# Kernel optimization log

Measured on AMD Instinct MI355X. Metric: run time of the kernel, lower is better.

Reference implementation:

```python
import jax, jax.numpy as jnp
import numpy as np

MARGIN = 1.0
EPS = 1e-08


def setup_inputs() -> dict:
    key = jax.random.key(0)
    k0, k1 = jax.random.split(key)
    kernels0 = jax.random.normal(k0, (2048, 3, 3), dtype=jnp.float32)
    kernels1 = jax.random.normal(k1, (1024, 5, 5), dtype=jnp.float32)
    return {"kernels0": kernels0, "kernels1": kernels1}


def _layer_loss(kernels):
    n, d, _ = kernels.shape
    # Frobenius-normalize each kernel
    norms = jnp.sqrt(jnp.sum(kernels * kernels, axis=(1, 2), keepdims=True)) + EPS
    kn = kernels / norms                      # (n, d, d)
    inv = jnp.linalg.inv(kn)                  # (n, d, d)
    # AB[i, j] = inv[i] @ kn[j]; BA[i, j] = inv[j] @ kn[i]
    ab = jnp.einsum('iab,jbc->ijac', inv, kn)  # (n, n, d, d)
    ba = jnp.einsum('jab,ibc->ijac', inv, kn)  # (n, n, d, d)
    eye = jnp.eye(d, dtype=kernels.dtype)
    diff_ab = jnp.sqrt(jnp.sum((eye - ab) ** 2, axis=(2, 3)))  # (n, n)
    diff_ba = jnp.sqrt(jnp.sum((eye - ba) ** 2, axis=(2, 3)))  # (n, n)
    combined = jnp.tril(diff_ab) + jnp.triu(diff_ba)
    loss_mat = jax.nn.relu(MARGIN - combined)
    mask = ~jnp.eye(n, dtype=bool)
    loss_mat = jnp.where(mask, loss_mat, 0.0)
    return jnp.sum(loss_mat) / (n * (n - 1))


def reference(kernels0, kernels1):
    losses = [_layer_loss(kernels0), _layer_loss(kernels1)]
    return sum(losses) / len(losses)
```

## Files before the change

kernel.cpp:

```cpp
#include <hip/hip_runtime.h>
#include <math.h>

#define N0 2048
#define N1 1024
#define M0T 32
#define M1T 32
#define NB0 (M0T * (M0T + 1) / 2)
#define NB1 (M1T * (M1T + 1) / 2)
#define NBLK0 (2 * NB0)
#define NBLK1 (2 * NB1)
#define NBTOT (NBLK0 + NBLK1)


__global__ __launch_bounds__(64) void prep_kernel(const float* __restrict__ k0,
                                                  const float* __restrict__ k1,
                                                  float* __restrict__ kn0,
                                                  float* __restrict__ inv0,
                                                  float* __restrict__ kn1,
                                                  float* __restrict__ inv1) {
    int t = blockIdx.x * blockDim.x + threadIdx.x;
    if (t < N0) {
        float a[9];
        float ss = 0.0f;
#pragma unroll
        for (int e = 0; e < 9; ++e) { a[e] = k0[t * 9 + e]; ss = fmaf(a[e], a[e], ss); }
        float rn = 1.0f / (sqrtf(ss) + 1e-8f);
#pragma unroll
        for (int e = 0; e < 9; ++e) a[e] *= rn;
        float c00 = a[4] * a[8] - a[5] * a[7];
        float c01 = -(a[3] * a[8] - a[5] * a[6]);
        float c02 = a[3] * a[7] - a[4] * a[6];
        float det = a[0] * c00 + a[1] * c01 + a[2] * c02;
        float id = 1.0f / det;
        float x[9];
        x[0] = c00 * id;
        x[1] = (a[2] * a[7] - a[1] * a[8]) * id;
        x[2] = (a[1] * a[5] - a[2] * a[4]) * id;
        x[3] = c01 * id;
        x[4] = (a[0] * a[8] - a[2] * a[6]) * id;
        x[5] = (a[2] * a[3] - a[0] * a[5]) * id;
        x[6] = c02 * id;
        x[7] = (a[1] * a[6] - a[0] * a[7]) * id;
        x[8] = (a[0] * a[4] - a[1] * a[3]) * id;
        float r[9];
#pragma unroll
        for (int i = 0; i < 3; ++i)
#pragma unroll
            for (int j = 0; j < 3; ++j) {
                float m = a[i * 3 + 0] * x[0 * 3 + j];
                m = fmaf(a[i * 3 + 1], x[1 * 3 + j], m);
                m = fmaf(a[i * 3 + 2], x[2 * 3 + j], m);
                r[i * 3 + j] = ((i == j) ? 2.0f : 0.0f) - m;
            }
        float xn[9];
#pragma unroll
        for (int i = 0; i < 3; ++i)
#pragma unroll
            for (int j = 0; j < 3; ++j) {
                float m = x[i * 3 + 0] * r[0 * 3 + j];
                m = fmaf(x[i * 3 + 1], r[1 * 3 + j], m);
                m = fmaf(x[i * 3 + 2], r[2 * 3 + j], m);
                xn[i * 3 + j] = m;
            }
#pragma unroll
        for (int e = 0; e < 9; ++e) {
            kn0[t * 9 + e] = a[e];
            inv0[t * 9 + e] = xn[e];
        }
    } else {
        int u = t - N0;
        if (u < N1) {
            float A[5][5], B[5][5], K[5][5];
            float ss = 0.0f;
#pragma unroll
            for (int r = 0; r < 5; ++r)
#pragma unroll
                for (int c = 0; c < 5; ++c) {
                    float v = k1[u * 25 + r * 5 + c];
                    A[r][c] = v;
                    ss = fmaf(v, v, ss);
                }
            float rn = 1.0f / (sqrtf(ss) + 1e-8f);
#pragma unroll
            for (int r = 0; r < 5; ++r)
#pragma unroll
                for (int c = 0; c < 5; ++c) {
                    A[r][c] *= rn;
                    K[r][c] = A[r][c];
                    kn1[u * 25 + r * 5 + c] = A[r][c];
                    B[r][c] = (r == c) ? 1.0f : 0.0f;
                }
#pragma unroll
            for (int k = 0; k < 5; ++k) {
#pragma unroll
                for (int r = k + 1; r < 5; ++r) {
                    bool sw = fabsf(A[r][k]) > fabsf(A[k][k]);
#pragma unroll
                    for (int c = k; c < 5; ++c) {
                        float Ar = A[r][c], Ak = A[k][c];
                        A[r][c] = sw ? Ak : Ar;
                        A[k][c] = sw ? Ar : Ak;
                    }
#pragma unroll
                    for (int c = 0; c < 5; ++c) {
                        float Br = B[r][c], Bk = B[k][c];
                        B[r][c] = sw ? Bk : Br;
                        B[k][c] = sw ? Br : Bk;
                    }
                }
                float piv = 1.0f / A[k][k];
#pragma unroll
                for (int c = k; c < 5; ++c) A[k][c] *= piv;
#pragma unroll
                for (int c = 0; c < 5; ++c) B[k][c] *= piv;
#pragma unroll
                for (int r = 0; r < 5; ++r) {
                    if (r == k) continue;
                    float f = A[r][k];
#pragma unroll
                    for (int c = k; c < 5; ++c) A[r][c] = fmaf(-f, A[k][c], A[r][c]);
#pragma unroll
                    for (int c = 0; c < 5; ++c) B[r][c] = fmaf(-f, B[k][c], B[r][c]);
                }
            }
            float R[5][5];
#pragma unroll
            for (int i = 0; i < 5; ++i)
#pragma unroll
                for (int j = 0; j < 5; ++j) {
                    float m = K[i][0] * B[0][j];
#pragma unroll
                    for (int k = 1; k < 5; ++k) m = fmaf(K[i][k], B[k][j], m);
                    R[i][j] = ((i == j) ? 2.0f : 0.0f) - m;
                }
#pragma unroll
            for (int i = 0; i < 5; ++i)
#pragma unroll
                for (int j = 0; j < 5; ++j) {
                    float m = B[i][0] * R[0][j];
#pragma unroll
                    for (int k = 1; k < 5; ++k) m = fmaf(B[i][k], R[k][j], m);
                    inv1[u * 25 + i * 5 + j] = m;
                }
        }
    }
}

__device__ __forceinline__ void tri_decode(int t, int& bi, int& bj) {
    int b = (int)((sqrtf(8.0f * t + 1.0f) - 1.0f) * 0.5f);
    while ((b + 1) * (b + 2) / 2 <= t) ++b;
    while (b * (b + 1) / 2 > t) --b;
    bi = b;
    bj = t - b * (b + 1) / 2;
}

__global__ __launch_bounds__(256) void pairs_kernel(const float* __restrict__ inv0,
                                                    const float* __restrict__ kn0,
                                                    const float* __restrict__ inv1,
                                                    const float* __restrict__ kn1,
                                                    float* __restrict__ partial) {
    __shared__ __align__(16) float sA[800];
    __shared__ __align__(16) float sB[400];
    int tid = threadIdx.x;
    float contrib = 0.0f;

    if (blockIdx.x < NBLK0) {
        int t = blockIdx.x;
        int pb = t >> 1, h = t & 1;
        int bi, bj;
        tri_decode(pb, bi, bj);

        const float4* gA = (const float4*)(inv0 + bi * 576);
        const float4* gB = (const float4*)(kn0 + bj * 576 + h * 288);
        if (tid < 216) {
            if (tid < 144) ((float4*)sA)[tid] = gA[tid];
            else ((float4*)sB)[tid - 144] = gB[tid - 144];
        }
        __syncthreads();

        int ti = tid >> 4, tj = tid & 15;
        int ibase = bi * 64 + ti * 4;
        int jbase = bj * 64 + h * 32 + tj * 2;
        float a[4][9];
#pragma unroll
        for (int u = 0; u < 4; ++u)
#pragma unroll
            for (int e = 0; e < 9; ++e) a[u][e] = sA[(ti * 4 + u) * 9 + e];
#pragma unroll
        for (int v = 0; v < 2; ++v) {
            float b[9];
#pragma unroll
            for (int e = 0; e < 9; ++e) b[e] = sB[(tj * 2 + v) * 9 + e];
#pragma unroll
            for (int u = 0; u < 4; ++u) {
                float s = 0.0f;
#pragma unroll
                for (int r = 0; r < 3; ++r)
#pragma unroll
                    for (int c = 0; c < 3; ++c) {
                        float m = a[u][r * 3 + 0] * b[c];
                        m = fmaf(a[u][r * 3 + 1], b[3 + c], m);
                        m = fmaf(a[u][r * 3 + 2], b[6 + c], m);
                        float d = ((r == c) ? 1.0f : 0.0f) - m;
                        s = fmaf(d, d, s);
                    }
                bool take = ((ibase + u) > (jbase + v)) && (s < 1.0f);
                contrib += take ? (1.0f - __builtin_amdgcn_sqrtf(s)) : 0.0f;
            }
        }
    } else {
        int t = blockIdx.x - NBLK0;
        int pb = t >> 1, h = t & 1;
        int bi, bj;
        tri_decode(pb, bi, bj);

        const float4* gA = (const float4*)(inv1 + bi * 800);
        const float4* gB = (const float4*)(kn1 + (bj * 32 + h * 16) * 25);
        for (int e = tid; e < 300; e += 256) {
            if (e < 200) ((float4*)sA)[e] = gA[e];
            else ((float4*)sB)[e - 200] = gB[e - 200];
        }
        __syncthreads();

        int ti = tid >> 4, tj = tid & 15;
        int ibase = bi * 32 + ti * 2;
        int j = bj * 32 + h * 16 + tj;
        float a[2][25];
#pragma unroll
        for (int u = 0; u < 2; ++u)
#pragma unroll
            for (int e = 0; e < 25; ++e) a[u][e] = sA[(ti * 2 + u) * 25 + e];
        float b[25];
#pragma unroll
        for (int e = 0; e < 25; ++e) b[e] = sB[tj * 25 + e];
#pragma unroll
        for (int u = 0; u < 2; ++u) {
            float s = 0.0f;
#pragma unroll
            for (int r = 0; r < 5; ++r)
#pragma unroll
                for (int c = 0; c < 5; ++c) {
                    float m = a[u][r * 5 + 0] * b[c];
#pragma unroll
                    for (int k = 1; k < 5; ++k) m = fmaf(a[u][r * 5 + k], b[k * 5 + c], m);
                    float d = ((r == c) ? 1.0f : 0.0f) - m;
                    s = fmaf(d, d, s);
                }
            bool take = ((ibase + u) > j) && (s < 1.0f);
            contrib += take ? (1.0f - __builtin_amdgcn_sqrtf(s)) : 0.0f;
        }
    }

#pragma unroll
    for (int off = 32; off; off >>= 1) contrib += __shfl_down(contrib, off);
    __shared__ float wsum[4];
    if ((tid & 63) == 0) wsum[tid >> 6] = contrib;
    __syncthreads();
    if (tid == 0) partial[blockIdx.x] = wsum[0] + wsum[1] + wsum[2] + wsum[3];
}

__global__ void finalize_kernel(const float* __restrict__ partial, float* __restrict__ out) {
    int tid = threadIdx.x;
    double s0 = 0.0, s1 = 0.0;
    for (int x = tid; x < NBLK0; x += 256) s0 += (double)partial[x];
    for (int x = NBLK0 + tid; x < NBTOT; x += 256) s1 += (double)partial[x];
#pragma unroll
    for (int off = 32; off; off >>= 1) {
        s0 += __shfl_down(s0, off);
        s1 += __shfl_down(s1, off);
    }
    __shared__ double w0[4], w1[4];
    if ((tid & 63) == 0) { w0[tid >> 6] = s0; w1[tid >> 6] = s1; }
    __syncthreads();
    if (tid == 0) {
        double S0 = w0[0] + w0[1] + w0[2] + w0[3];
        double S1 = w1[0] + w1[1] + w1[2] + w1[3];
        double res = S0 / ((double)N0 * (double)(N0 - 1)) +
                     S1 / ((double)N1 * (double)(N1 - 1));
        out[0] = (float)res;
    }
}

extern "C" void kernel_launch(void* const* d_in, const int* in_sizes, int n_in,
                              void* d_out, int out_size, void* d_ws, size_t ws_size,
                              hipStream_t stream) {
    const float* k0 = (const float*)d_in[0];
    const float* k1 = (const float*)d_in[1];
    float* out = (float*)d_out;

    float* ws = (float*)d_ws;
    float* kn0 = ws;
    float* inv0 = kn0 + N0 * 9;
    float* kn1 = inv0 + N0 * 9;
    float* inv1 = kn1 + N1 * 25;
    float* partial = inv1 + N1 * 25;

    int totalPrep = N0 + N1;
    prep_kernel<<<(totalPrep + 63) / 64, 64, 0, stream>>>(k0, k1, kn0, inv0, kn1, inv1);
    pairs_kernel<<<NBTOT, 256, 0, stream>>>(inv0, kn0, inv1, kn1, partial);
    finalize_kernel<<<1, 256, 0, stream>>>(partial, out);
}
```

Baseline: 69.82 us.

## Fuse normalization and inversion prep into the pairwise kernel, dropping prep launch

Removes the separate prep kernel and computes per-kernel normalization and inverse inside each pairs block while it loads its tiles into shared memory. This removes one kernel launch and the global round-trip for the normalized and inverted matrices. In exchange, every tile's inverses are recomputed redundantly by each block that uses them, and only a subset of threads does that serial inversion work before the barrier, which lengthens each block's prologue.

```diff
diff --git a/kernel.cpp b/kernel.cpp
--- a/kernel.cpp
+++ b/kernel.cpp
@@ -12,140 +12,6 @@
 #define NBTOT (NBLK0 + NBLK1)
 
 
-__global__ __launch_bounds__(64) void prep_kernel(const float* __restrict__ k0,
-                                                  const float* __restrict__ k1,
-                                                  float* __restrict__ kn0,
-                                                  float* __restrict__ inv0,
-                                                  float* __restrict__ kn1,
-                                                  float* __restrict__ inv1) {
-    int t = blockIdx.x * blockDim.x + threadIdx.x;
-    if (t < N0) {
-        float a[9];
-        float ss = 0.0f;
-#pragma unroll
-        for (int e = 0; e < 9; ++e) { a[e] = k0[t * 9 + e]; ss = fmaf(a[e], a[e], ss); }
-        float rn = 1.0f / (sqrtf(ss) + 1e-8f);
-#pragma unroll
-        for (int e = 0; e < 9; ++e) a[e] *= rn;
-        float c00 = a[4] * a[8] - a[5] * a[7];
-        float c01 = -(a[3] * a[8] - a[5] * a[6]);
-        float c02 = a[3] * a[7] - a[4] * a[6];
-        float det = a[0] * c00 + a[1] * c01 + a[2] * c02;
-        float id = 1.0f / det;
-        float x[9];
-        x[0] = c00 * id;
-        x[1] = (a[2] * a[7] - a[1] * a[8]) * id;
-        x[2] = (a[1] * a[5] - a[2] * a[4]) * id;
-        x[3] = c01 * id;
-        x[4] = (a[0] * a[8] - a[2] * a[6]) * id;
-        x[5] = (a[2] * a[3] - a[0] * a[5]) * id;
-        x[6] = c02 * id;
-        x[7] = (a[1] * a[6] - a[0] * a[7]) * id;
-        x[8] = (a[0] * a[4] - a[1] * a[3]) * id;
-        float r[9];
-#pragma unroll
-        for (int i = 0; i < 3; ++i)
-#pragma unroll
-            for (int j = 0; j < 3; ++j) {
-                float m = a[i * 3 + 0] * x[0 * 3 + j];
-                m = fmaf(a[i * 3 + 1], x[1 * 3 + j], m);
-                m = fmaf(a[i * 3 + 2], x[2 * 3 + j], m);
-                r[i * 3 + j] = ((i == j) ? 2.0f : 0.0f) - m;
-            }
-        float xn[9];
-#pragma unroll
-        for (int i = 0; i < 3; ++i)
-#pragma unroll
-            for (int j = 0; j < 3; ++j) {
-                float m = x[i * 3 + 0] * r[0 * 3 + j];
-                m = fmaf(x[i * 3 + 1], r[1 * 3 + j], m);
-                m = fmaf(x[i * 3 + 2], r[2 * 3 + j], m);
-                xn[i * 3 + j] = m;
-            }
-#pragma unroll
-        for (int e = 0; e < 9; ++e) {
-            kn0[t * 9 + e] = a[e];
-            inv0[t * 9 + e] = xn[e];
-        }
-    } else {
-        int u = t - N0;
-        if (u < N1) {
-            float A[5][5], B[5][5], K[5][5];
-            float ss = 0.0f;
-#pragma unroll
-            for (int r = 0; r < 5; ++r)
-#pragma unroll
-                for (int c = 0; c < 5; ++c) {
-                    float v = k1[u * 25 + r * 5 + c];
-                    A[r][c] = v;
-                    ss = fmaf(v, v, ss);
-                }
-            float rn = 1.0f / (sqrtf(ss) + 1e-8f);
-#pragma unroll
-            for (int r = 0; r < 5; ++r)
-#pragma unroll
-                for (int c = 0; c < 5; ++c) {
-                    A[r][c] *= rn;
-                    K[r][c] = A[r][c];
-                    kn1[u * 25 + r * 5 + c] = A[r][c];
-                    B[r][c] = (r == c) ? 1.0f : 0.0f;
-                }
-#pragma unroll
-            for (int k = 0; k < 5; ++k) {
-#pragma unroll
-                for (int r = k + 1; r < 5; ++r) {
-                    bool sw = fabsf(A[r][k]) > fabsf(A[k][k]);
-#pragma unroll
-                    for (int c = k; c < 5; ++c) {
-                        float Ar = A[r][c], Ak = A[k][c];
-                        A[r][c] = sw ? Ak : Ar;
-                        A[k][c] = sw ? Ar : Ak;
-                    }
-#pragma unroll
-                    for (int c = 0; c < 5; ++c) {
-                        float Br = B[r][c], Bk = B[k][c];
-                        B[r][c] = sw ? Bk : Br;
-                        B[k][c] = sw ? Br : Bk;
-                    }
-                }
-                float piv = 1.0f / A[k][k];
-#pragma unroll
-                for (int c = k; c < 5; ++c) A[k][c] *= piv;
-#pragma unroll
-                for (int c = 0; c < 5; ++c) B[k][c] *= piv;
-#pragma unroll
-                for (int r = 0; r < 5; ++r) {
-                    if (r == k) continue;
-                    float f = A[r][k];
-#pragma unroll
-                    for (int c = k; c < 5; ++c) A[r][c] = fmaf(-f, A[k][c], A[r][c]);
-#pragma unroll
-                    for (int c = 0; c < 5; ++c) B[r][c] = fmaf(-f, B[k][c], B[r][c]);
-                }
-            }
-            float R[5][5];
-#pragma unroll
-            for (int i = 0; i < 5; ++i)
-#pragma unroll
-                for (int j = 0; j < 5; ++j) {
-                    float m = K[i][0] * B[0][j];
-#pragma unroll
-                    for (int k = 1; k < 5; ++k) m = fmaf(K[i][k], B[k][j], m);
-                    R[i][j] = ((i == j) ? 2.0f : 0.0f) - m;
-                }
-#pragma unroll
-            for (int i = 0; i < 5; ++i)
-#pragma unroll
-                for (int j = 0; j < 5; ++j) {
-                    float m = B[i][0] * R[0][j];
-#pragma unroll
-                    for (int k = 1; k < 5; ++k) m = fmaf(B[i][k], R[k][j], m);
-                    inv1[u * 25 + i * 5 + j] = m;
-                }
-        }
-    }
-}
-
 __device__ __forceinline__ void tri_decode(int t, int& bi, int& bj) {
     int b = (int)((sqrtf(8.0f * t + 1.0f) - 1.0f) * 0.5f);
     while ((b + 1) * (b + 2) / 2 <= t) ++b;
@@ -154,10 +20,146 @@
     bj = t - b * (b + 1) / 2;
 }
 
-__global__ __launch_bounds__(256) void pairs_kernel(const float* __restrict__ inv0,
-                                                    const float* __restrict__ kn0,
-                                                    const float* __restrict__ inv1,
-                                                    const float* __restrict__ kn1,
+__device__ __forceinline__ void inv3_to(const float* __restrict__ g, float* __restrict__ dst) {
+    float a[9];
+    float ss = 0.0f;
+#pragma unroll
+    for (int e = 0; e < 9; ++e) { a[e] = g[e]; ss = fmaf(a[e], a[e], ss); }
+    float rn = 1.0f / (sqrtf(ss) + 1e-8f);
+#pragma unroll
+    for (int e = 0; e < 9; ++e) a[e] *= rn;
+    float c00 = a[4] * a[8] - a[5] * a[7];
+    float c01 = -(a[3] * a[8] - a[5] * a[6]);
+    float c02 = a[3] * a[7] - a[4] * a[6];
+    float det = a[0] * c00 + a[1] * c01 + a[2] * c02;
+    float id = 1.0f / det;
+    float x[9];
+    x[0] = c00 * id;
+    x[1] = (a[2] * a[7] - a[1] * a[8]) * id;
+    x[2] = (a[1] * a[5] - a[2] * a[4]) * id;
+    x[3] = c01 * id;
+    x[4] = (a[0] * a[8] - a[2] * a[6]) * id;
+    x[5] = (a[2] * a[3] - a[0] * a[5]) * id;
+    x[6] = c02 * id;
+    x[7] = (a[1] * a[6] - a[0] * a[7]) * id;
+    x[8] = (a[0] * a[4] - a[1] * a[3]) * id;
+    float r[9];
+#pragma unroll
+    for (int i = 0; i < 3; ++i)
+#pragma unroll
+        for (int j = 0; j < 3; ++j) {
+            float m = a[i * 3 + 0] * x[0 * 3 + j];
+            m = fmaf(a[i * 3 + 1], x[1 * 3 + j], m);
+            m = fmaf(a[i * 3 + 2], x[2 * 3 + j], m);
+            r[i * 3 + j] = ((i == j) ? 2.0f : 0.0f) - m;
+        }
+#pragma unroll
+    for (int i = 0; i < 3; ++i)
+#pragma unroll
+        for (int j = 0; j < 3; ++j) {
+            float m = x[i * 3 + 0] * r[0 * 3 + j];
+            m = fmaf(x[i * 3 + 1], r[1 * 3 + j], m);
+            m = fmaf(x[i * 3 + 2], r[2 * 3 + j], m);
+            dst[i * 3 + j] = m;
+        }
+}
+
+__device__ __forceinline__ void norm3_to(const float* __restrict__ g, float* __restrict__ dst) {
+    float a[9];
+    float ss = 0.0f;
+#pragma unroll
+    for (int e = 0; e < 9; ++e) { a[e] = g[e]; ss = fmaf(a[e], a[e], ss); }
+    float rn = 1.0f / (sqrtf(ss) + 1e-8f);
+#pragma unroll
+    for (int e = 0; e < 9; ++e) dst[e] = a[e] * rn;
+}
+
+__device__ __forceinline__ void inv5_to(const float* __restrict__ g, float* __restrict__ dst) {
+    float A[5][5], B[5][5], K[5][5];
+    float ss = 0.0f;
+#pragma unroll
+    for (int r = 0; r < 5; ++r)
+#pragma unroll
+        for (int c = 0; c < 5; ++c) {
+            float v = g[r * 5 + c];
+            A[r][c] = v;
+            ss = fmaf(v, v, ss);
+        }
+    float rn = 1.0f / (sqrtf(ss) + 1e-8f);
+#pragma unroll
+    for (int r = 0; r < 5; ++r)
+#pragma unroll
+        for (int c = 0; c < 5; ++c) {
+            A[r][c] *= rn;
+            K[r][c] = A[r][c];
+            B[r][c] = (r == c) ? 1.0f : 0.0f;
+        }
+#pragma unroll
+    for (int k = 0; k < 5; ++k) {
+#pragma unroll
+        for (int r = k + 1; r < 5; ++r) {
+            bool sw = fabsf(A[r][k]) > fabsf(A[k][k]);
+#pragma unroll
+            for (int c = k; c < 5; ++c) {
+                float Ar = A[r][c], Ak = A[k][c];
+                A[r][c] = sw ? Ak : Ar;
+                A[k][c] = sw ? Ar : Ak;
+            }
+#pragma unroll
+            for (int c = 0; c < 5; ++c) {
+                float Br = B[r][c], Bk = B[k][c];
+                B[r][c] = sw ? Bk : Br;
+                B[k][c] = sw ? Br : Bk;
+            }
+        }
+        float piv = 1.0f / A[k][k];
+#pragma unroll
+        for (int c = k; c < 5; ++c) A[k][c] *= piv;
+#pragma unroll
+        for (int c = 0; c < 5; ++c) B[k][c] *= piv;
+#pragma unroll
+        for (int r = 0; r < 5; ++r) {
+            if (r == k) continue;
+            float f = A[r][k];
+#pragma unroll
+            for (int c = k; c < 5; ++c) A[r][c] = fmaf(-f, A[k][c], A[r][c]);
+#pragma unroll
+            for (int c = 0; c < 5; ++c) B[r][c] = fmaf(-f, B[k][c], B[r][c]);
+        }
+    }
+    float R[5][5];
+#pragma unroll
+    for (int i = 0; i < 5; ++i)
+#pragma unroll
+        for (int j = 0; j < 5; ++j) {
+            float m = K[i][0] * B[0][j];
+#pragma unroll
+            for (int k = 1; k < 5; ++k) m = fmaf(K[i][k], B[k][j], m);
+            R[i][j] = ((i == j) ? 2.0f : 0.0f) - m;
+        }
+#pragma unroll
+    for (int i = 0; i < 5; ++i)
+#pragma unroll
+        for (int j = 0; j < 5; ++j) {
+            float m = B[i][0] * R[0][j];
+#pragma unroll
+            for (int k = 1; k < 5; ++k) m = fmaf(B[i][k], R[k][j], m);
+            dst[i * 5 + j] = m;
+        }
+}
+
+__device__ __forceinline__ void norm5_to(const float* __restrict__ g, float* __restrict__ dst) {
+    float a[25];
+    float ss = 0.0f;
+#pragma unroll
+    for (int e = 0; e < 25; ++e) { a[e] = g[e]; ss = fmaf(a[e], a[e], ss); }
+    float rn = 1.0f / (sqrtf(ss) + 1e-8f);
+#pragma unroll
+    for (int e = 0; e < 25; ++e) dst[e] = a[e] * rn;
+}
+
+__global__ __launch_bounds__(256) void pairs_kernel(const float* __restrict__ k0,
+                                                    const float* __restrict__ k1,
                                                     float* __restrict__ partial) {
     __shared__ __align__(16) float sA[800];
     __shared__ __align__(16) float sB[400];
@@ -170,11 +172,11 @@
         int bi, bj;
         tri_decode(pb, bi, bj);
 
-        const float4* gA = (const float4*)(inv0 + bi * 576);
-        const float4* gB = (const float4*)(kn0 + bj * 576 + h * 288);
-        if (tid < 216) {
-            if (tid < 144) ((float4*)sA)[tid] = gA[tid];
-            else ((float4*)sB)[tid - 144] = gB[tid - 144];
+        if (tid < 64) {
+            inv3_to(k0 + (bi * 64 + tid) * 9, sA + tid * 9);
+        } else if (tid < 96) {
+            int j = tid - 64;
+            norm3_to(k0 + (bj * 64 + h * 32 + j) * 9, sB + j * 9);
         }
         __syncthreads();
 
@@ -214,11 +216,11 @@
         int bi, bj;
         tri_decode(pb, bi, bj);
 
-        const float4* gA = (const float4*)(inv1 + bi * 800);
-        const float4* gB = (const float4*)(kn1 + (bj * 32 + h * 16) * 25);
-        for (int e = tid; e < 300; e += 256) {
-            if (e < 200) ((float4*)sA)[e] = gA[e];
-            else ((float4*)sB)[e - 200] = gB[e - 200];
+        if (tid < 32) {
+            inv5_to(k1 + (bi * 32 + tid) * 25, sA + tid * 25);
+        } else if (tid < 48) {
+            int j = tid - 32;
+            norm5_to(k1 + (bj * 32 + h * 16 + j) * 25, sB + j * 25);
         }
         __syncthreads();
 
@@ -288,15 +290,8 @@
     const float* k1 = (const float*)d_in[1];
     float* out = (float*)d_out;
 
-    float* ws = (float*)d_ws;
-    float* kn0 = ws;
-    float* inv0 = kn0 + N0 * 9;
-    float* kn1 = inv0 + N0 * 9;
-    float* inv1 = kn1 + N1 * 25;
-    float* partial = inv1 + N1 * 25;
-
-    int totalPrep = N0 + N1;
-    prep_kernel<<<(totalPrep + 63) / 64, 64, 0, stream>>>(k0, k1, kn0, inv0, kn1, inv1);
-    pairs_kernel<<<NBTOT, 256, 0, stream>>>(inv0, kn0, inv1, kn1, partial);
+    float* partial = (float*)d_ws;
+
+    pairs_kernel<<<NBTOT, 256, 0, stream>>>(k0, k1, partial);
     finalize_kernel<<<1, 256, 0, stream>>>(partial, out);
 }
```

After: 69.91 us. Within noise of the previous version (+0.1%).
